# Performance work log

Hardware: AMD Instinct MI355X
Metric: run time of the kernel (lower is better)

Reference implementation:

```python
import jax, jax.numpy as jnp
import numpy as np

DT = 0.01
SIGMA_RECUR = 0.005
SIGMA_INPUT = 0.05


def setup_inputs() -> dict:
    key = jax.random.key(0)
    ks = jax.random.split(key, 13)
    B, T, I, H = 64, 1000, 4, 512
    H2 = 2 * H
    return {
        "inp": jax.random.normal(ks[0], (B, T, I), jnp.float32),
        "hn": jax.random.uniform(ks[1], (1, B, H2), jnp.float32),
        "x": jax.random.normal(ks[2], (1, B, H2), jnp.float32),
        "inhib_stim": jax.random.normal(ks[3], (B, H2), jnp.float32),
        "perturb_hid": jax.random.normal(ks[4], (T,), jnp.float32),
        "perturb_inp": jax.random.normal(ks[5], (T,), jnp.float32),
        "str2str": jax.random.uniform(ks[6], (H, H), jnp.float32, -0.01, 0.01),
        "alm2alm": jax.random.uniform(ks[7], (H, H), jnp.float32, -0.01, 0.01),
        "alm2str": jax.random.uniform(ks[8], (H, H), jnp.float32, -0.01, 0.01),
        "str2alm": jax.random.uniform(ks[9], (H, H), jnp.float32, -0.01, 0.01),
        "inp_weight": jax.random.uniform(ks[10], (I, H2), jnp.float32, -0.01, 0.01),
        "fc1_w": jax.random.uniform(ks[11], (1, H2), jnp.float32, -0.03, 0.03),
        "fc1_b": jnp.zeros((1,), jnp.float32),
    }


def reference(inp, hn, x, inhib_stim, perturb_hid, perturb_inp,
              str2str, alm2alm, alm2str, str2alm, inp_weight, fc1_w, fc1_b):
    H = str2str.shape[0]
    # W_rec: [[str2str, alm2str], [str2alm, alm2alm]] -> (2H, 2H)
    W_rec = jnp.concatenate([
        jnp.concatenate([str2str, alm2str], axis=1),
        jnp.concatenate([str2alm, alm2alm], axis=1),
    ], axis=0)
    str_mask = jnp.concatenate([jnp.ones((H,), inp.dtype), jnp.zeros((H,), inp.dtype)])
    alm_mask = jnp.concatenate([jnp.zeros((H,), inp.dtype), jnp.ones((H,), inp.dtype)])

    # scalar per-step noise, as in the original (single Normal draw per t)
    ph = jnp.sqrt(2 * DT * SIGMA_RECUR ** 2) * perturb_hid  # [T]
    pi = jnp.sqrt(2 * DT * SIGMA_INPUT ** 2) * perturb_inp  # [T]

    h0 = hn[0]  # [B, 2H]
    x0 = x[0]   # [B, 2H]

    def step(carry, xs_t):
        h_prev, x_prev = carry
        inp_t, ph_t, pi_t = xs_t  # inp_t: [B, I]
        drive = (inp_t + pi_t) @ inp_weight  # [B, 2H]
        x_new = x_prev + DT * (-x_prev + h_prev @ W_rec.T
                               + drive * str_mask + inhib_stim) + ph_t
        h_new = jax.nn.relu(x_new)
        return (h_new, x_new), (h_new, x_new)

    inp_t_major = jnp.transpose(inp, (1, 0, 2))  # [T, B, I]
    (_, _), (hs, xs) = jax.lax.scan(step, (h0, x0), (inp_t_major, ph, pi))

    rnn_out = jnp.transpose(hs, (1, 0, 2))  # [B, T, 2H]
    x_out = jnp.transpose(xs, (1, 0, 2))    # [B, T, 2H]
    hn_last = rnn_out[:, -1, :][None]       # [1, B, 2H]
    x_last = x_out[:, -1, :][None]
    out = (rnn_out * alm_mask) @ fc1_w.T + fc1_b  # [B, T, 1]
    return (out, hn_last, rnn_out, x_last, x_out)
```

## Files before the change

kernel.cpp:

```cpp
#include <hip/hip_runtime.h>
#include <hip/hip_bf16.h>

#define TT 1000
#define HH 512
#define HH2 1024
#define DT_ 0.01f
#define PH_SCALE 7.0710678118654745e-4f
#define PI_SCALE 7.0710678118654745e-3f

typedef short s16x8 __attribute__((ext_vector_type(8)));
typedef float f32x4 __attribute__((ext_vector_type(4)));
typedef unsigned u32x4 __attribute__((ext_vector_type(4)));

#define SIGN32  0x80008000u
#define STRIP32 0x7fff7fffu

static __device__ __forceinline__ unsigned short bf16_bits(float f) {
    union { __hip_bfloat16 h; unsigned short u; } b; b.h = __float2bfloat16(f); return b.u;
}
static __device__ __forceinline__ unsigned pat32(int t) {
    const unsigned tg = ((unsigned)t >> 1) & 3u;
    return ((tg & 1u) << 15) | ((tg & 2u) << 30);
}

__global__ __launch_bounds__(256, 1) void rnn_persistent(
    const float* __restrict__ inp, const float* __restrict__ hn,
    const float* __restrict__ x0g, const float* __restrict__ inhib,
    const float* __restrict__ ph, const float* __restrict__ pig,
    const float* __restrict__ s2s, const float* __restrict__ a2a,
    const float* __restrict__ a2s, const float* __restrict__ s2a,
    const float* __restrict__ iw,
    float* __restrict__ rnn_out, float* __restrict__ x_out,
    unsigned* __restrict__ hbuf)
{
    const int tid  = threadIdx.x;
    const int wid  = tid >> 6;
    const int lane = tid & 63;
    const int b    = blockIdx.x;
    const int g    = b >> 4;
    const int qb   = b & 15;
    const int l15  = lane & 15;
    const int lq   = lane >> 4;
    const int r4   = l15 & 3;
    const int g4   = g * 4;
    const int icol = (qb * 4 + wid) * 16 + l15;
    const bool owner = (lq == 0);

    __shared__ __align__(16) unsigned short hlds[2][4 * 1024];

    {
        float h0v[4];
        #pragma unroll
        for (int r = 0; r < 4; ++r)
            h0v[r] = hn[(size_t)(g4 + r) * HH2 + icol];
        float prr[4];
        #pragma unroll
        for (int r = 0; r < 4; ++r) prr[r] = __shfl_xor(h0v[r], 1);
        if (owner && !(l15 & 1)) {
            const unsigned p0 = pat32(0);
            #pragma unroll
            for (int r = 0; r < 4; ++r) {
                const unsigned val = (((unsigned)bf16_bits(h0v[r]) |
                                       ((unsigned)bf16_bits(prr[r]) << 16)) & STRIP32);
                __hip_atomic_store(hbuf + (size_t)(g4 + r) * 512 + (icol >> 1),
                                   val | p0, __ATOMIC_RELAXED, __HIP_MEMORY_SCOPE_AGENT);
            }
        }
    }

    s16x8 wfr[32];
    #pragma unroll
    for (int kc = 0; kc < 32; ++kc) {
        const int j = kc * 32 + lq * 8;
        const float* src;
        if (icol < HH) src = (j < HH) ? (s2s + (size_t)icol * HH + j)
                                      : (a2s + (size_t)icol * HH + (j - HH));
        else           src = (j < HH) ? (s2a + (size_t)(icol - HH) * HH + j)
                                      : (a2a + (size_t)(icol - HH) * HH + (j - HH));
        const float4 f0 = *(const float4*)(src);
        const float4 f1 = *(const float4*)(src + 4);
        union { s16x8 vv; unsigned short us[8]; } u;
        u.us[0] = bf16_bits(f0.x); u.us[1] = bf16_bits(f0.y);
        u.us[2] = bf16_bits(f0.z); u.us[3] = bf16_bits(f0.w);
        u.us[4] = bf16_bits(f1.x); u.us[5] = bf16_bits(f1.y);
        u.us[6] = bf16_bits(f1.z); u.us[7] = bf16_bits(f1.w);
        wfr[kc] = u.vv;
    }

    const bool isStr = (icol < HH);
    float iw0 = 0.f, iw1 = 0.f, iw2 = 0.f, iw3 = 0.f;
    if (isStr) {
        iw0 = iw[icol]; iw1 = iw[HH2 + icol];
        iw2 = iw[2 * HH2 + icol]; iw3 = iw[3 * HH2 + icol];
    }
    float xr[4], inh[4];
    float4 ipf[4];
    #pragma unroll
    for (int r = 0; r < 4; ++r) {
        const int bi = g4 + r;
        xr[r]  = x0g[(size_t)bi * HH2 + icol];
        inh[r] = inhib[(size_t)bi * HH2 + icol];
        ipf[r] = *(const float4*)(inp + ((size_t)bi * TT + 0) * 4);
    }
    float phv = ph[0], piv = pig[0];

    auto stage = [&](int t) {
        const unsigned* srcs = hbuf + (size_t)(t & 1) * 32768 + (size_t)g4 * 512;
        char* dst = (char*)hlds[t & 1];
        const unsigned p32 = pat32(t);
        const int row0 = tid >> 7,         c160 = tid & 127;
        const int row1 = (tid + 256) >> 7, c161 = tid & 127;
        const unsigned* p0 = srcs + row0 * 512 + c160 * 4;
        const unsigned* p1 = srcs + row1 * 512 + c161 * 4;
        char* d0 = dst + (c160 * 4 + row0) * 16;
        char* d1 = dst + (c161 * 4 + row1) * 16;
        u32x4 c0, c1;
        asm volatile("global_load_dwordx4 %0, %1, off sc0 sc1" : "=v"(c0) : "v"(p0) : "memory");
        asm volatile("global_load_dwordx4 %0, %1, off sc0 sc1" : "=v"(c1) : "v"(p1) : "memory");
        asm volatile("s_waitcnt vmcnt(1)" ::: "memory");
        bool f0 = (((c0[0] ^ p32) | (c0[1] ^ p32) | (c0[2] ^ p32) | (c0[3] ^ p32)) & SIGN32) != 0u;
        if (!f0) { u32x4 s = {c0[0] & STRIP32, c0[1] & STRIP32, c0[2] & STRIP32, c0[3] & STRIP32};
                   *(u32x4*)d0 = s; }
        asm volatile("s_waitcnt vmcnt(0)" ::: "memory");
        bool f1 = (((c1[0] ^ p32) | (c1[1] ^ p32) | (c1[2] ^ p32) | (c1[3] ^ p32)) & SIGN32) != 0u;
        if (!f1) { u32x4 s = {c1[0] & STRIP32, c1[1] & STRIP32, c1[2] & STRIP32, c1[3] & STRIP32};
                   *(u32x4*)d1 = s; }
        float burn = (float)tid;
        while (f0 || f1) {
            if (f0) asm volatile("global_load_dwordx4 %0, %1, off sc0 sc1" : "=v"(c0) : "v"(p0) : "memory");
            if (f1) asm volatile("global_load_dwordx4 %0, %1, off sc0 sc1" : "=v"(c1) : "v"(p1) : "memory");
            #pragma unroll
            for (int z = 0; z < 8; ++z) burn = fmaf(burn, 1.000001f, 0.5f);
            asm volatile("" :: "v"(burn));
            asm volatile("s_waitcnt vmcnt(0)" ::: "memory");
            if (f0 && ((((c0[0] ^ p32) | (c0[1] ^ p32) | (c0[2] ^ p32) | (c0[3] ^ p32)) & SIGN32) == 0u)) {
                u32x4 s = {c0[0] & STRIP32, c0[1] & STRIP32, c0[2] & STRIP32, c0[3] & STRIP32};
                *(u32x4*)d0 = s; f0 = false;
            }
            if (f1 && ((((c1[0] ^ p32) | (c1[1] ^ p32) | (c1[2] ^ p32) | (c1[3] ^ p32)) & SIGN32) == 0u)) {
                u32x4 s = {c1[0] & STRIP32, c1[1] & STRIP32, c1[2] & STRIP32, c1[3] & STRIP32};
                *(u32x4*)d1 = s; f1 = false;
            }
        }
    };

    stage(0);
    __syncthreads();

    #pragma unroll 1
    for (int t = 0; t < TT; ++t) {
        f32x4 acc[4] = {{0,0,0,0},{0,0,0,0},{0,0,0,0},{0,0,0,0}};
        const char* arow = (const char*)hlds[t & 1] + (lq * 4 + r4) * 16;
        #pragma unroll
        for (int kc = 0; kc < 32; ++kc) {
            s16x8 a0 = *(const s16x8*)(arow + kc * 256);
            acc[kc & 3] = __builtin_amdgcn_mfma_f32_16x16x32_bf16(a0, wfr[kc], acc[kc & 3], 0, 0, 0);
        }

        const float phs = PH_SCALE * phv;
        const float pis = PI_SCALE * piv;
        float xn_[4], hv_[4];
        #pragma unroll
        for (int r = 0; r < 4; ++r) {
            const float rec = acc[0][r] + acc[1][r] + acc[2][r] + acc[3][r];
            float drive = 0.f;
            if (isStr) drive = (ipf[r].x + pis) * iw0 + (ipf[r].y + pis) * iw1 +
                               (ipf[r].z + pis) * iw2 + (ipf[r].w + pis) * iw3;
            const float xp = xr[r];
            const float xn = xp + DT_ * (-xp + rec + drive + inh[r]) + phs;
            const float hv = fmaxf(xn, 0.f);
            xr[r] = xn; xn_[r] = xn; hv_[r] = hv;
        }

        if (t + 1 < TT) {
            unsigned* nxt = hbuf + (size_t)((t + 1) & 1) * 32768;
            const unsigned pn = pat32(t + 1);
            float prr[4];
            #pragma unroll
            for (int r = 0; r < 4; ++r) prr[r] = __shfl_xor(hv_[r], 1);
            if (owner && !(l15 & 1)) {
                #pragma unroll
                for (int r = 0; r < 4; ++r) {
                    const unsigned val = (((unsigned)bf16_bits(hv_[r]) |
                                           ((unsigned)bf16_bits(prr[r]) << 16)) & STRIP32);
                    __hip_atomic_store(nxt + (size_t)(g4 + r) * 512 + (icol >> 1),
                                       val | pn, __ATOMIC_RELAXED, __HIP_MEMORY_SCOPE_AGENT);
                }
            }
        }

        if (owner) {
            #pragma unroll
            for (int r = 0; r < 4; ++r) {
                const int bi = g4 + r;
                const size_t o = ((size_t)bi * TT + t) * HH2 + icol;
                rnn_out[o] = hv_[r];
                x_out[o]   = xn_[r];
            }
        }

        const int tn = (t + 1 < TT) ? (t + 1) : t;
        #pragma unroll
        for (int r = 0; r < 4; ++r)
            ipf[r] = *(const float4*)(inp + ((size_t)(g4 + r) * TT + tn) * 4);
        phv = ph[tn]; piv = pig[tn];

        if (t + 1 < TT) stage(t + 1);
        __syncthreads();
    }
}

__global__ __launch_bounds__(256) void fc1_kernel(
    const float* __restrict__ rnn_out, const float* __restrict__ fc1_w,
    const float* __restrict__ fc1_b, float* __restrict__ out)
{
    const int wid = blockIdx.x * 4 + (threadIdx.x >> 6);
    const int lane = threadIdx.x & 63;
    const float* p = rnn_out + (size_t)wid * HH2 + HH + lane * 8;
    const float* w = fc1_w + HH + lane * 8;
    f32x4 v0 = *(const f32x4*)(p);
    f32x4 v1 = *(const f32x4*)(p + 4);
    f32x4 w0 = *(const f32x4*)(w);
    f32x4 w1 = *(const f32x4*)(w + 4);
    float s = v0[0]*w0[0] + v0[1]*w0[1] + v0[2]*w0[2] + v0[3]*w0[3]
            + v1[0]*w1[0] + v1[1]*w1[1] + v1[2]*w1[2] + v1[3]*w1[3];
    #pragma unroll
    for (int off = 32; off; off >>= 1) s += __shfl_xor(s, off);
    if (lane == 0) out[wid] = s + fc1_b[0];
}

__global__ __launch_bounds__(256) void last_kernel(
    const float* __restrict__ rnn_out, const float* __restrict__ x_out,
    float* __restrict__ hn_last, float* __restrict__ x_last)
{
    const int idx = blockIdx.x * 256 + threadIdx.x;
    const int b = idx >> 10;
    const int i = idx & 1023;
    const size_t o = ((size_t)b * TT + (TT - 1)) * HH2 + i;
    hn_last[idx] = rnn_out[o];
    x_last[idx]  = x_out[o];
}

extern "C" void kernel_launch(void* const* d_in, const int* in_sizes, int n_in,
                              void* d_out, int out_size, void* d_ws, size_t ws_size,
                              hipStream_t stream) {
    const float* inp   = (const float*)d_in[0];
    const float* hn    = (const float*)d_in[1];
    const float* x     = (const float*)d_in[2];
    const float* inhib = (const float*)d_in[3];
    const float* ph    = (const float*)d_in[4];
    const float* pi    = (const float*)d_in[5];
    const float* s2s   = (const float*)d_in[6];
    const float* a2a   = (const float*)d_in[7];
    const float* a2s   = (const float*)d_in[8];
    const float* s2a   = (const float*)d_in[9];
    const float* iw    = (const float*)d_in[10];
    const float* fw    = (const float*)d_in[11];
    const float* fb    = (const float*)d_in[12];

    float* out     = (float*)d_out;
    float* hn_last = out + 64000;
    float* rnn_out = out + 129536;
    float* x_last  = out + 65665536;
    float* x_out   = out + 65731072;

    unsigned* hbuf = (unsigned*)d_ws;

    rnn_persistent<<<256, 256, 0, stream>>>(inp, hn, x, inhib, ph, pi,
                                            s2s, a2a, a2s, s2a, iw,
                                            rnn_out, x_out, hbuf);
    fc1_kernel<<<16000, 256, 0, stream>>>(rnn_out, fw, fb, out);
    last_kernel<<<256, 256, 0, stream>>>(rnn_out, x_out, hn_last, x_last);
}
```

Baseline: 2.068 ms.

## Poll peer hidden state via L2 first, swizzle LDS slots, remap blocks

Every hidden-state publish now writes twice: once with sc0 (visible in L2) and once with sc0 sc1 (system coherent). Consumers first spin with sc0-only loads, on the expectation that producers on the same XCD share L2. Only after a bounded number of rounds do they fall back to sc1 loads, and if that fallback happens after the first steps, sc1 is used from then on. The change also XOR-swizzles the LDS slot layout to cut bank conflicts on the MFMA A-operand reads, and swaps the block-index mapping so each batch group's blocks are spread across XCDs differently. The cost is extra store traffic from the double publish, and relying on L2-visible polling adds some risk around cross-XCD coherence timing.

```diff
diff --git a/kernel.cpp b/kernel.cpp
--- a/kernel.cpp
+++ b/kernel.cpp
@@ -14,6 +14,7 @@
 
 #define SIGN32  0x80008000u
 #define STRIP32 0x7fff7fffu
+#define SC0_BOUND 24
 
 static __device__ __forceinline__ unsigned short bf16_bits(float f) {
     union { __hip_bfloat16 h; unsigned short u; } b; b.h = __float2bfloat16(f); return b.u;
@@ -22,6 +23,7 @@
     const unsigned tg = ((unsigned)t >> 1) & 3u;
     return ((tg & 1u) << 15) | ((tg & 2u) << 30);
 }
+static __device__ __forceinline__ int ldslot(int j) { return j ^ ((j >> 3) & 7); }
 
 __global__ __launch_bounds__(256, 1) void rnn_persistent(
     const float* __restrict__ inp, const float* __restrict__ hn,
@@ -37,8 +39,8 @@
     const int wid  = tid >> 6;
     const int lane = tid & 63;
     const int b    = blockIdx.x;
-    const int g    = b >> 4;
-    const int qb   = b & 15;
+    const int g    = b & 15;
+    const int qb   = b >> 4;
     const int l15  = lane & 15;
     const int lq   = lane >> 4;
     const int r4   = l15 & 3;
@@ -47,6 +49,11 @@
     const bool owner = (lq == 0);
 
     __shared__ __align__(16) unsigned short hlds[2][4 * 1024];
+
+    auto pub = [&](unsigned* p, unsigned v) {
+        asm volatile("global_store_dword %0, %1, off sc0"     :: "v"(p), "v"(v) : "memory");
+        asm volatile("global_store_dword %0, %1, off sc0 sc1" :: "v"(p), "v"(v) : "memory");
+    };
 
     {
         float h0v[4];
@@ -62,8 +69,7 @@
             for (int r = 0; r < 4; ++r) {
                 const unsigned val = (((unsigned)bf16_bits(h0v[r]) |
                                        ((unsigned)bf16_bits(prr[r]) << 16)) & STRIP32);
-                __hip_atomic_store(hbuf + (size_t)(g4 + r) * 512 + (icol >> 1),
-                                   val | p0, __ATOMIC_RELAXED, __HIP_MEMORY_SCOPE_AGENT);
+                pub(hbuf + (size_t)(g4 + r) * 512 + (icol >> 1), val | p0);
             }
         }
     }
@@ -104,6 +110,8 @@
     }
     float phv = ph[0], piv = pig[0];
 
+    bool l3m = false;
+
     auto stage = [&](int t) {
         const unsigned* srcs = hbuf + (size_t)(t & 1) * 32768 + (size_t)g4 * 512;
         char* dst = (char*)hlds[t & 1];
@@ -112,34 +120,57 @@
         const int row1 = (tid + 256) >> 7, c161 = tid & 127;
         const unsigned* p0 = srcs + row0 * 512 + c160 * 4;
         const unsigned* p1 = srcs + row1 * 512 + c161 * 4;
-        char* d0 = dst + (c160 * 4 + row0) * 16;
-        char* d1 = dst + (c161 * 4 + row1) * 16;
+        char* d0 = dst + ldslot(c160 * 4 + row0) * 16;
+        char* d1 = dst + ldslot(c161 * 4 + row1) * 16;
         u32x4 c0, c1;
-        asm volatile("global_load_dwordx4 %0, %1, off sc0 sc1" : "=v"(c0) : "v"(p0) : "memory");
-        asm volatile("global_load_dwordx4 %0, %1, off sc0 sc1" : "=v"(c1) : "v"(p1) : "memory");
-        asm volatile("s_waitcnt vmcnt(1)" ::: "memory");
-        bool f0 = (((c0[0] ^ p32) | (c0[1] ^ p32) | (c0[2] ^ p32) | (c0[3] ^ p32)) & SIGN32) != 0u;
-        if (!f0) { u32x4 s = {c0[0] & STRIP32, c0[1] & STRIP32, c0[2] & STRIP32, c0[3] & STRIP32};
-                   *(u32x4*)d0 = s; }
-        asm volatile("s_waitcnt vmcnt(0)" ::: "memory");
-        bool f1 = (((c1[0] ^ p32) | (c1[1] ^ p32) | (c1[2] ^ p32) | (c1[3] ^ p32)) & SIGN32) != 0u;
-        if (!f1) { u32x4 s = {c1[0] & STRIP32, c1[1] & STRIP32, c1[2] & STRIP32, c1[3] & STRIP32};
-                   *(u32x4*)d1 = s; }
+        bool f0 = true, f1 = true;
         float burn = (float)tid;
-        while (f0 || f1) {
-            if (f0) asm volatile("global_load_dwordx4 %0, %1, off sc0 sc1" : "=v"(c0) : "v"(p0) : "memory");
-            if (f1) asm volatile("global_load_dwordx4 %0, %1, off sc0 sc1" : "=v"(c1) : "v"(p1) : "memory");
-            #pragma unroll
-            for (int z = 0; z < 8; ++z) burn = fmaf(burn, 1.000001f, 0.5f);
-            asm volatile("" :: "v"(burn));
+
+        if (!l3m) {
+            asm volatile("global_load_dwordx4 %0, %1, off sc0" : "=v"(c0) : "v"(p0) : "memory");
+            asm volatile("global_load_dwordx4 %0, %1, off sc0" : "=v"(c1) : "v"(p1) : "memory");
+            asm volatile("s_waitcnt vmcnt(1)" ::: "memory");
+            f0 = (((c0[0] ^ p32) | (c0[1] ^ p32) | (c0[2] ^ p32) | (c0[3] ^ p32)) & SIGN32) != 0u;
+            if (!f0) { u32x4 s = {c0[0] & STRIP32, c0[1] & STRIP32, c0[2] & STRIP32, c0[3] & STRIP32};
+                       *(u32x4*)d0 = s; }
             asm volatile("s_waitcnt vmcnt(0)" ::: "memory");
-            if (f0 && ((((c0[0] ^ p32) | (c0[1] ^ p32) | (c0[2] ^ p32) | (c0[3] ^ p32)) & SIGN32) == 0u)) {
-                u32x4 s = {c0[0] & STRIP32, c0[1] & STRIP32, c0[2] & STRIP32, c0[3] & STRIP32};
-                *(u32x4*)d0 = s; f0 = false;
-            }
-            if (f1 && ((((c1[0] ^ p32) | (c1[1] ^ p32) | (c1[2] ^ p32) | (c1[3] ^ p32)) & SIGN32) == 0u)) {
-                u32x4 s = {c1[0] & STRIP32, c1[1] & STRIP32, c1[2] & STRIP32, c1[3] & STRIP32};
-                *(u32x4*)d1 = s; f1 = false;
+            f1 = (((c1[0] ^ p32) | (c1[1] ^ p32) | (c1[2] ^ p32) | (c1[3] ^ p32)) & SIGN32) != 0u;
+            if (!f1) { u32x4 s = {c1[0] & STRIP32, c1[1] & STRIP32, c1[2] & STRIP32, c1[3] & STRIP32};
+                       *(u32x4*)d1 = s; }
+            for (int rnd = 0; (f0 || f1) && rnd < SC0_BOUND; ++rnd) {
+                if (f0) asm volatile("global_load_dwordx4 %0, %1, off sc0" : "=v"(c0) : "v"(p0) : "memory");
+                if (f1) asm volatile("global_load_dwordx4 %0, %1, off sc0" : "=v"(c1) : "v"(p1) : "memory");
+                #pragma unroll
+                for (int z = 0; z < 8; ++z) burn = fmaf(burn, 1.000001f, 0.5f);
+                asm volatile("" :: "v"(burn));
+                asm volatile("s_waitcnt vmcnt(0)" ::: "memory");
+                if (f0 && ((((c0[0] ^ p32) | (c0[1] ^ p32) | (c0[2] ^ p32) | (c0[3] ^ p32)) & SIGN32) == 0u)) {
+                    u32x4 s = {c0[0] & STRIP32, c0[1] & STRIP32, c0[2] & STRIP32, c0[3] & STRIP32};
+                    *(u32x4*)d0 = s; f0 = false;
+                }
+                if (f1 && ((((c1[0] ^ p32) | (c1[1] ^ p32) | (c1[2] ^ p32) | (c1[3] ^ p32)) & SIGN32) == 0u)) {
+                    u32x4 s = {c1[0] & STRIP32, c1[1] & STRIP32, c1[2] & STRIP32, c1[3] & STRIP32};
+                    *(u32x4*)d1 = s; f1 = false;
+                }
+            }
+        }
+        if (f0 || f1) {
+            if (t >= 4) l3m = true;
+            while (f0 || f1) {
+                if (f0) asm volatile("global_load_dwordx4 %0, %1, off sc0 sc1" : "=v"(c0) : "v"(p0) : "memory");
+                if (f1) asm volatile("global_load_dwordx4 %0, %1, off sc0 sc1" : "=v"(c1) : "v"(p1) : "memory");
+                #pragma unroll
+                for (int z = 0; z < 8; ++z) burn = fmaf(burn, 1.000001f, 0.5f);
+                asm volatile("" :: "v"(burn));
+                asm volatile("s_waitcnt vmcnt(0)" ::: "memory");
+                if (f0 && ((((c0[0] ^ p32) | (c0[1] ^ p32) | (c0[2] ^ p32) | (c0[3] ^ p32)) & SIGN32) == 0u)) {
+                    u32x4 s = {c0[0] & STRIP32, c0[1] & STRIP32, c0[2] & STRIP32, c0[3] & STRIP32};
+                    *(u32x4*)d0 = s; f0 = false;
+                }
+                if (f1 && ((((c1[0] ^ p32) | (c1[1] ^ p32) | (c1[2] ^ p32) | (c1[3] ^ p32)) & SIGN32) == 0u)) {
+                    u32x4 s = {c1[0] & STRIP32, c1[1] & STRIP32, c1[2] & STRIP32, c1[3] & STRIP32};
+                    *(u32x4*)d1 = s; f1 = false;
+                }
             }
         }
     };
@@ -150,10 +181,11 @@
     #pragma unroll 1
     for (int t = 0; t < TT; ++t) {
         f32x4 acc[4] = {{0,0,0,0},{0,0,0,0},{0,0,0,0},{0,0,0,0}};
-        const char* arow = (const char*)hlds[t & 1] + (lq * 4 + r4) * 16;
+        const char* base = (const char*)hlds[t & 1];
+        const int vbase = lq * 4 + r4;
         #pragma unroll
         for (int kc = 0; kc < 32; ++kc) {
-            s16x8 a0 = *(const s16x8*)(arow + kc * 256);
+            s16x8 a0 = *(const s16x8*)(base + ldslot(kc * 16 + vbase) * 16);
             acc[kc & 3] = __builtin_amdgcn_mfma_f32_16x16x32_bf16(a0, wfr[kc], acc[kc & 3], 0, 0, 0);
         }
 
@@ -183,8 +215,7 @@
                 for (int r = 0; r < 4; ++r) {
                     const unsigned val = (((unsigned)bf16_bits(hv_[r]) |
                                            ((unsigned)bf16_bits(prr[r]) << 16)) & STRIP32);
-                    __hip_atomic_store(nxt + (size_t)(g4 + r) * 512 + (icol >> 1),
-                                       val | pn, __ATOMIC_RELAXED, __HIP_MEMORY_SCOPE_AGENT);
+                    pub(nxt + (size_t)(g4 + r) * 512 + (icol >> 1), val | pn);
                 }
             }
         }
```

Result: slower. 7.211 ms (+248.7%).
